# Kernel optimization log

Hardware: AMD Instinct MI355X
Metric: run time of the kernel (lower is better)

The kernel has to match this reference:

```python
import jax, jax.numpy as jnp
import numpy as np
from jax import lax

NMS_THRESHOLD = 0.45
PRE_THRESHOLD = 0.005


def setup_inputs() -> dict:
    key = jax.random.key(0)
    k1, k2 = jax.random.split(key)
    B, C, N = 8, 20, 2048
    u = jax.random.uniform(k1, (B, N, 4), dtype=jnp.float32)  # raw rand per spec
    # build valid [x1,y1,x2,y2] boxes from raw uniforms (center + size param)
    cx, cy = u[..., 0], u[..., 1]
    w = u[..., 2] * 0.2 + 0.01
    h = u[..., 3] * 0.2 + 0.01
    bbs = jnp.stack([cx - w / 2, cy - h / 2, cx + w / 2, cy + h / 2], axis=-1)
    conf = jax.random.uniform(k2, (B, C, N), dtype=jnp.float32)
    return {"bbs": bbs, "conf": conf}


def _nms_filter(bbs, conf, nms_threshold, pre_threshold):
    # bbs: [B, N, 4] (x1,y1,x2,y2); conf: [B, C, N]
    B, C, N = conf.shape
    order = jnp.argsort(-conf, axis=-1)                      # [B,C,N] desc by score
    conf_s = jnp.take_along_axis(conf, order, axis=-1)       # sorted scores
    boxes_b = jnp.broadcast_to(bbs[:, None, :, :], (B, C, N, 4))
    boxes_s = jnp.take_along_axis(boxes_b, order[..., None], axis=2)  # [B,C,N,4]

    x1, y1, x2, y2 = (boxes_s[..., i] for i in range(4))
    areas = jnp.maximum(x2 - x1, 0.0) * jnp.maximum(y2 - y1, 0.0)     # [B,C,N]
    pos = jnp.arange(N)

    keep0 = conf_s > pre_threshold  # pre-threshold: dropped boxes never kept nor suppress

    def body(i, keep):
        # box at sorted rank i
        bx1 = lax.dynamic_index_in_dim(x1, i, 2, keepdims=True)  # [B,C,1]
        by1 = lax.dynamic_index_in_dim(y1, i, 2, keepdims=True)
        bx2 = lax.dynamic_index_in_dim(x2, i, 2, keepdims=True)
        by2 = lax.dynamic_index_in_dim(y2, i, 2, keepdims=True)
        a_i = lax.dynamic_index_in_dim(areas, i, 2, keepdims=True)
        iw = jnp.maximum(jnp.minimum(bx2, x2) - jnp.maximum(bx1, x1), 0.0)
        ih = jnp.maximum(jnp.minimum(by2, y2) - jnp.maximum(by1, y1), 0.0)
        inter = iw * ih
        iou = inter / jnp.maximum(a_i + areas - inter, 1e-12)    # [B,C,N]
        keep_i = lax.dynamic_index_in_dim(keep, i, 2, keepdims=True)  # alive pivot?
        suppress = (iou > nms_threshold) & (pos > i) & keep_i
        return keep & ~suppress

    keep = lax.fori_loop(0, N, body, keep0)
    filt_s = conf_s * keep.astype(conf_s.dtype)
    inv = jnp.argsort(order, axis=-1)                          # inverse permutation
    return jnp.take_along_axis(filt_s, inv, axis=-1)


def reference(bbs, conf):
    return _nms_filter(bbs, conf, NMS_THRESHOLD, PRE_THRESHOLD)
```

## Files before the change

### kernel.cpp

```cpp
#include <hip/hip_runtime.h>


#define BB   8
#define CC   20
#define NBOX 2048
#define CAP  64
#define PRE_THR 0.005f
#define IOU_M 0x1.CCCCCDp-2

typedef unsigned long long u64;
typedef unsigned int u32;
typedef unsigned short u16;

__device__ u32 g_deg[BB * NBOX];
__device__ u16 g_nbr[(size_t)BB * NBOX * CAP];

__device__ __forceinline__ float area_rn(float x1, float y1, float x2, float y2) {
    return __fmul_rn(fmaxf(__fsub_rn(x2, x1), 0.f), fmaxf(__fsub_rn(y2, y1), 0.f));
}
__device__ __forceinline__ bool iou_gt(float inter, float den) {
    return (double)inter > IOU_M * (double)den;
}

__global__ __launch_bounds__(1024) void adj_kernel(const float4* __restrict__ bbs) {
    const int batch = blockIdx.x >> 5;
    const int seg   = blockIdx.x & 31;
    const int lane  = threadIdx.x & 63;
    const int wv    = threadIdx.x >> 6;

    __shared__ float4 sbox[NBOX];
    __shared__ float  sar[NBOX];

    const float4* bp = bbs + (size_t)batch * NBOX;
    for (int n = threadIdx.x; n < NBOX; n += 1024) {
        float4 bv = bp[n];
        sbox[n] = bv;
        sar[n]  = area_rn(bv.x, bv.y, bv.z, bv.w);
    }
    __syncthreads();

    const int r0 = seg * 64 + wv * 4;
    float4 rb[4]; float ra[4]; u32 hits[4] = {0, 0, 0, 0};
    #pragma unroll
    for (int t = 0; t < 4; ++t) { rb[t] = sbox[r0 + t]; ra[t] = sar[r0 + t]; }

    #pragma unroll 4
    for (int k = 0; k < 32; ++k) {
        const int c = lane + (k << 6);
        const float4 cb = sbox[c];
        const float  ca = sar[c];
        #pragma unroll
        for (int t = 0; t < 4; ++t) {
            float iw = fmaxf(__fsub_rn(fminf(rb[t].z, cb.z), fmaxf(rb[t].x, cb.x)), 0.f);
            float ih = fmaxf(__fsub_rn(fminf(rb[t].w, cb.w), fmaxf(rb[t].y, cb.y)), 0.f);
            float inter = __fmul_rn(iw, ih);
            float den = fmaxf(__fsub_rn(__fadd_rn(ra[t], ca), inter), 1e-12f);
            if (c != r0 + t && iou_gt(inter, den)) hits[t] |= 1u << k;
        }
    }

    #pragma unroll
    for (int t = 0; t < 4; ++t) {
        const int i = r0 + t;
        int cnt = __popc(hits[t]);
        int ofs = cnt;
        #pragma unroll
        for (int d = 1; d < 64; d <<= 1) {
            int v = __shfl_up(ofs, d);
            if (lane >= d) ofs += v;
        }
        int total = __shfl(ofs, 63);
        ofs -= cnt;
        u16* row = g_nbr + ((size_t)batch * NBOX + i) * CAP;
        u32 h = hits[t];
        while (h) {
            int k = __ffs(h) - 1; h &= h - 1;
            if (ofs < CAP) row[ofs] = (u16)(lane + (k << 6));
            ++ofs;
        }
        if (lane == 0) g_deg[batch * NBOX + i] = (u32)min(total, CAP);
    }
}

__global__ __launch_bounds__(256) void prop_kernel(const float* __restrict__ conf,
                                                   float* __restrict__ out) {
    const int wg   = blockIdx.x;
    const int b    = wg / CC;
    const int base = wg * NBOX;
    const int tid  = threadIdx.x;

    __shared__ u64           skey[NBOX];
    __shared__ unsigned char sstate[NBOX];
    __shared__ int sflag;

    const u32* degb = g_deg + b * NBOX;
    const u16* nbrb = g_nbr + (size_t)b * NBOX * CAP;

    float cv[8]; u32 dreg[8]; u32 und = 0;
    #pragma unroll
    for (int p = 0; p < 8; ++p) {
        const int i = tid + (p << 8);
        float c = conf[base + i];
        cv[p] = c;
        dreg[p] = degb[i];
        skey[i] = ((u64)__float_as_uint(c) << 32) | (u32)(~i);
        bool live = (c > PRE_THR);
        sstate[i] = live ? 0 : 2;
        if (live) und |= 1u << p;
    }
    if (tid == 0) sflag = 0;
    __syncthreads();

    while (true) {
        bool changed = false;
        u32 m = und;
        while (m) {
            const int p = __ffs(m) - 1; m &= m - 1;
            const int i = tid + (p << 8);
            const u64 ki = skey[i];
            const int d  = (int)dreg[p];
            const u16* row = nbrb + (size_t)i * CAP;
            int verdict = 1;
            for (int e = 0; e < d; ++e) {
                const int j = row[e];
                if (skey[j] > ki) {
                    const int st = sstate[j];
                    if (st == 1) { verdict = 2; break; }
                    if (st == 0) verdict = 0;
                }
            }
            if (verdict != 0) {
                sstate[i] = (unsigned char)verdict;
                und &= ~(1u << p);
                changed = true;
            }
        }
        if (changed) sflag = 1;
        __syncthreads();
        const int f = sflag;
        __syncthreads();
        if (!f) break;
        if (tid == 0) sflag = 0;
        __syncthreads();
    }

    #pragma unroll
    for (int p = 0; p < 8; ++p) {
        const int i = tid + (p << 8);
        out[base + i] = (sstate[i] == 1) ? cv[p] : 0.f;
    }
}

extern "C" void kernel_launch(void* const* d_in, const int* in_sizes, int n_in,
                              void* d_out, int out_size, void* d_ws, size_t ws_size,
                              hipStream_t stream) {
    const float* bbs  = (const float*)d_in[0];
    const float* conf = (const float*)d_in[1];
    float* out = (float*)d_out;
    (void)d_ws; (void)ws_size;

    adj_kernel<<<dim3(BB * 32), dim3(1024), 0, stream>>>((const float4*)bbs);
    prop_kernel<<<dim3(BB * CC), dim3(256), 0, stream>>>(conf, out);
}
```

Measured before the change: 110.0 us.

## Pack NMS state into sort key, cache first neighbors, single-barrier rounds

The propagation kernel now stores each box's state in the low two bits of its shared sort key, so one 64-bit shared load gives both rank and status. The first four neighbor indices are preloaded into registers, the key is kept in a register, and accepted bits are tracked in a register mask. Each round's termination check uses a monotonic round-number flag, cutting three barriers per round to one. The adjacency kernel moves the self-exclusion test out of the inner loop into a post-loop mask fix-up. The cost is higher register pressure from the extra per-thread arrays.

```diff
diff --git a/kernel.cpp b/kernel.cpp
--- a/kernel.cpp
+++ b/kernel.cpp
@@ -55,9 +55,12 @@
             float ih = fmaxf(__fsub_rn(fminf(rb[t].w, cb.w), fmaxf(rb[t].y, cb.y)), 0.f);
             float inter = __fmul_rn(iw, ih);
             float den = fmaxf(__fsub_rn(__fadd_rn(ra[t], ca), inter), 1e-12f);
-            if (c != r0 + t && iou_gt(inter, den)) hits[t] |= 1u << k;
+            if (iou_gt(inter, den)) hits[t] |= 1u << k;
         }
     }
+    #pragma unroll
+    for (int t = 0; t < 4; ++t)
+        if (lane == ((wv << 2) + t)) hits[t] &= ~(1u << seg);
 
     #pragma unroll
     for (int t = 0; t < 4; ++t) {
@@ -89,65 +92,66 @@
     const int base = wg * NBOX;
     const int tid  = threadIdx.x;
 
-    __shared__ u64           skey[NBOX];
-    __shared__ unsigned char sstate[NBOX];
+    __shared__ u64 skey[NBOX];
     __shared__ int sflag;
 
     const u32* degb = g_deg + b * NBOX;
     const u16* nbrb = g_nbr + (size_t)b * NBOX * CAP;
 
-    float cv[8]; u32 dreg[8]; u32 und = 0;
+    float cv[8]; u32 dreg[8]; u64 nb4[8]; u64 kreg[8];
+    u32 und = 0, abits = 0;
     #pragma unroll
     for (int p = 0; p < 8; ++p) {
         const int i = tid + (p << 8);
         float c = conf[base + i];
-        cv[p] = c;
+        cv[p]   = c;
         dreg[p] = degb[i];
-        skey[i] = ((u64)__float_as_uint(c) << 32) | (u32)(~i);
+        nb4[p]  = *(const u64*)(nbrb + (size_t)i * CAP);
         bool live = (c > PRE_THR);
-        sstate[i] = live ? 0 : 2;
+        u64 key = ((u64)__float_as_uint(c) << 32) | ((u64)(u32)(2047 - i) << 2);
+        kreg[p] = key;
+        skey[i] = key | (live ? 0u : 2u);
         if (live) und |= 1u << p;
     }
     if (tid == 0) sflag = 0;
     __syncthreads();
 
-    while (true) {
+    for (int r = 1;; ++r) {
         bool changed = false;
-        u32 m = und;
-        while (m) {
-            const int p = __ffs(m) - 1; m &= m - 1;
-            const int i = tid + (p << 8);
-            const u64 ki = skey[i];
+        #pragma unroll
+        for (int p = 0; p < 8; ++p) {
+            if (!(und & (1u << p))) continue;
+            const int i  = tid + (p << 8);
+            const u64 ki = kreg[p];
             const int d  = (int)dreg[p];
-            const u16* row = nbrb + (size_t)i * CAP;
             int verdict = 1;
             for (int e = 0; e < d; ++e) {
-                const int j = row[e];
-                if (skey[j] > ki) {
-                    const int st = sstate[j];
-                    if (st == 1) { verdict = 2; break; }
-                    if (st == 0) verdict = 0;
+                const int j = (e < 4)
+                    ? (int)((nb4[p] >> (e * 16)) & 0xFFFF)
+                    : (int)nbrb[(size_t)i * CAP + e];
+                const u64 kj = skey[j];
+                if (kj > ki) {
+                    const u32 st = (u32)kj & 3u;
+                    if (st == 1u) { verdict = 2; break; }
+                    if (st == 0u) verdict = 0;
                 }
             }
             if (verdict != 0) {
-                sstate[i] = (unsigned char)verdict;
+                if (verdict == 1) abits |= 1u << p;
+                skey[i] = ki | (u32)verdict;
                 und &= ~(1u << p);
                 changed = true;
             }
         }
-        if (changed) sflag = 1;
+        if (changed) sflag = r;
         __syncthreads();
-        const int f = sflag;
-        __syncthreads();
-        if (!f) break;
-        if (tid == 0) sflag = 0;
-        __syncthreads();
+        if (sflag < r) break;
     }
 
     #pragma unroll
     for (int p = 0; p < 8; ++p) {
         const int i = tid + (p << 8);
-        out[base + i] = (sstate[i] == 1) ? cv[p] : 0.f;
+        out[base + i] = ((abits >> p) & 1u) ? cv[p] : 0.f;
     }
 }
 
```

New measurement: 100.5 us. 8.7% less time.
